# Optimization experiments

Measured on AMD Instinct MI355X. Metric: run time of the kernel, lower is better.

Reference implementation:

```python
import jax, jax.numpy as jnp
import numpy as np

VOCAB, D_MODEL, D_STATE, D_LATENT = 32000, 1024, 16, 32
SEQ, MAX_ITERS, TOL = 8192, 20, 1e-5


def _linear_params(k, out_d, in_d):
    lim = 1.0 / np.sqrt(in_d)  # eqx.nn.Linear default uniform init
    kw, kb = jax.random.split(k)
    W = jax.random.uniform(kw, (out_d, in_d), minval=-lim, maxval=lim, dtype=jnp.float32)
    b = jax.random.uniform(kb, (out_d,), minval=-lim, maxval=lim, dtype=jnp.float32)
    return W, b


def setup_inputs() -> dict:
    key = jax.random.key(0)
    ks = jax.random.split(key, 8)
    tokens = jax.random.randint(ks[0], (SEQ,), 0, VOCAB)
    emb = jax.random.normal(ks[1], (VOCAB, D_MODEL), dtype=jnp.float32) * 0.02
    Wf, bf = _linear_params(ks[2], D_LATENT // 2, D_STATE + D_MODEL)
    Wf2, bf2 = _linear_params(ks[3], D_LATENT // 2, D_STATE + D_MODEL)
    Wlam, blam = _linear_params(ks[4], D_STATE, D_LATENT + D_MODEL)
    Wu, bu = _linear_params(ks[5], D_STATE, D_LATENT + D_MODEL)
    Wout, bout = _linear_params(ks[6], D_MODEL, D_LATENT + D_STATE)
    return {"tokens": tokens, "emb": emb, "Wf": Wf, "bf": bf, "Wf2": Wf2, "bf2": bf2,
            "Wlam": Wlam, "blam": blam, "Wu": Wu, "bu": bu, "Wout": Wout, "bout": bout}


def reference(tokens, emb, Wf, bf, Wf2, bf2, Wlam, blam, Wu, bu, Wout, bout):
    x = emb[tokens]  # [S, d_model]

    def compute_lambda_u(z):
        zx = jnp.concatenate([z, x], axis=-1)              # [S, d_latent+d_model]
        lam = jax.nn.sigmoid(zx @ Wlam.T + blam)           # [S, d_state]
        u = zx @ Wu.T + bu                                 # [S, d_state]
        return lam, u

    def scan_h(lam, u):
        # h_t = lam_t * h_{t-1} + u_t via associative scan
        def binop(left, right):
            a1, b1 = left
            a2, b2 = right
            return (a1 * a2, a2 * b1 + b2)
        _, h = jax.lax.associative_scan(binop, (lam, u), axis=0)
        return h

    def f_theta(z, h_prev):
        hx = jnp.concatenate([h_prev, x], axis=-1)         # [S, d_state+d_model]
        alpha = jax.nn.sigmoid(hx @ Wf.T + bf)             # [S, d_latent//2]
        sigma = jax.nn.sigmoid(hx @ Wf2.T + bf2)
        u, v = jnp.split(z, 2, axis=-1)
        rho, beta, gamma = 30.0, 15.6, 0.26
        thresh = jnp.tanh(rho * (v - u))
        du = 1.0 - alpha * jnp.exp(beta * v) * (1.0 - gamma * (0.3 - u)) + sigma * thresh
        dv = -1.0 + alpha * jnp.exp(beta * u) * (1.0 + gamma * (0.3 - v)) + sigma * thresh
        return z + 0.001 * jnp.concatenate([du, dv], axis=-1)

    # Bounded fixed-point iteration with convergence freeze (emulates while_loop)
    def body(carry, _):
        z, z_prev, done = carry
        done = done | (jnp.linalg.norm(z - z_prev) < TOL)
        lam, u = compute_lambda_u(z)
        h = scan_h(lam, u)
        h_prev = jnp.concatenate([jnp.zeros((1, D_STATE), z.dtype), h[:-1]], axis=0)
        z_new = f_theta(z, h_prev)
        z_out = jnp.where(done, z, z_new)
        zp_out = jnp.where(done, z_prev, z)
        return (z_out, zp_out, done), None

    z0 = jnp.zeros((SEQ, D_LATENT), jnp.float32)
    zp0 = jnp.full((SEQ, D_LATENT), jnp.inf, jnp.float32)
    (z_star, _, _), _ = jax.lax.scan(body, (z0, zp0, jnp.array(False)), None, length=MAX_ITERS)

    lam, u = compute_lambda_u(z_star)
    h_star = scan_h(lam, u)
    zh = jnp.concatenate([z_star, h_star], axis=-1)        # [S, d_latent+d_state]
    return zh @ Wout.T + bout                              # [S, d_model]
```

## Files before the change

### kernel.cpp

```cpp
#include <hip/hip_runtime.h>

#define SEQ     8192
#define DM      1024
#define NB      256
#define CH      32
#define HALO    32
#define W       64
#define NT      1024
#define MAXITERS 20

__device__ __forceinline__ float sigmoidf(float x) {
    return 1.0f / (1.0f + __expf(-x));
}
__device__ __forceinline__ float tanh_fast(float x) {
    const float e = __expf(2.0f * x);
    return 1.0f - 2.0f / (e + 1.0f);
}
__device__ __forceinline__ float rl(float v, int lane) {
    return __uint_as_float(__builtin_amdgcn_readlane(__float_as_uint(v), lane));
}

__global__ __launch_bounds__(256) void k1_embed_proj(
    const int* __restrict__ tokens, const float* __restrict__ emb,
    const float* __restrict__ Wf,  const float* __restrict__ bf,
    const float* __restrict__ Wf2, const float* __restrict__ bf2,
    const float* __restrict__ Wlam,const float* __restrict__ blam,
    const float* __restrict__ Wu,  const float* __restrict__ bu,
    float* __restrict__ xlam, float* __restrict__ xu,
    float* __restrict__ xf,   float* __restrict__ xf2)
{
    __shared__ float4 xs4[8 * 256];
    const int tid = threadIdx.x;
    const int tokbase = blockIdx.x * 8;

    for (int j = tid; j < 8 * 256; j += 256) {
        const int tok = j >> 8, q = j & 255;
        const int row = tokens[tokbase + tok];
        const int qs = q ^ ((q >> 6) & 3);
        xs4[tok * 256 + qs] =
            *reinterpret_cast<const float4*>(emb + (size_t)row * DM + q * 4);
    }
    __syncthreads();

    const int r  = tid >> 2;
    const int kq = tid & 3;
    const int arr = r >> 4;
    const int c   = r & 15;

    const float* wb; const float* bv; float* dst; int wstr, woff;
    if (arr == 0)      { wb = Wlam; wstr = 1056; woff = 32; bv = blam; dst = xlam; }
    else if (arr == 1) { wb = Wu;   wstr = 1056; woff = 32; bv = bu;   dst = xu;   }
    else if (arr == 2) { wb = Wf;   wstr = 1040; woff = 16; bv = bf;   dst = xf;   }
    else               { wb = Wf2;  wstr = 1040; woff = 16; bv = bf2;  dst = xf2;  }

    const float4* wrow = reinterpret_cast<const float4*>(wb + (size_t)c * wstr + woff) + kq * 64;

    float2 a2[8];
    #pragma unroll
    for (int t = 0; t < 8; ++t) a2[t] = make_float2(0.f, 0.f);

    #pragma unroll 8
    for (int i = 0; i < 64; ++i) {
        const float4 w4 = wrow[i];
        const int gs = (kq * 64 + i) ^ kq;
        #pragma unroll
        for (int t = 0; t < 8; ++t) {
            const float4 x4 = xs4[t * 256 + gs];
            a2[t].x += w4.x * x4.x;  a2[t].y += w4.y * x4.y;
            a2[t].x += w4.z * x4.z;  a2[t].y += w4.w * x4.w;
        }
    }

    #pragma unroll
    for (int t = 0; t < 8; ++t) {
        float acc = a2[t].x + a2[t].y;
        acc += __shfl_xor(acc, 1);
        acc += __shfl_xor(acc, 2);
        if (kq == 0) {
            const float bz = bv[c];
            dst[(size_t)(tokbase + t) * 16 + c] = acc + bz;
        }
    }
}

__global__ __launch_bounds__(NT) void k2_fixed_point(
    const float* __restrict__ Wf,  const float* __restrict__ Wf2,
    const float* __restrict__ Wlam,const float* __restrict__ Wu,
    const float* __restrict__ xf,  const float* __restrict__ xf2,
    const float* __restrict__ xlam,const float* __restrict__ xu,
    const float* __restrict__ Wout,const float* __restrict__ bout,
    float* __restrict__ out)
{
    __shared__ float zsf[W * 32];
    __shared__ float hhT[16][W + 2];
    __shared__ float zhs[CH][48];

    const int tid = threadIdx.x;
    const int b = blockIdx.x;
    const int s0 = (b - 1) * CH;
    const int tl = tid & 63;
    const int c  = __builtin_amdgcn_readfirstlane(tid >> 6);

    for (int i = tid; i < W * 32; i += NT) zsf[i] = 0.0f;

    const float* WlamC = Wlam + (size_t)c * 1056;
    const float* WuC   = Wu   + (size_t)c * 1056;
    const float* WfC   = Wf   + (size_t)c * 1040;
    const float* Wf2C  = Wf2  + (size_t)c * 1040;
    const float w0 = (tl < 32) ? WlamC[tl] : WuC[tl - 32];
    const float w1 = (tl < 16) ? WfC[tl] : ((tl < 32) ? Wf2C[tl - 16] : 0.0f);

    const int gt = s0 + tl;
    const bool act = (gt >= 0);
    const size_t gi = (size_t)(act ? gt : 0) * 16 + c;
    const float xl = xlam[gi], xuv = xu[gi], xfv = xf[gi], x2v = xf2[gi];
    const int sw = tl & 7;
    __syncthreads();

    for (int r = 1; r <= MAXITERS + 1; ++r) {
        float accx = xl, accy = xuv;
        #pragma unroll
        for (int g = 0; g < 8; ++g) {
            const float4 z4 = *reinterpret_cast<const float4*>(
                &zsf[tl * 32 + ((g ^ sw) << 2)]);
            const int s0_ = 4 * g;
            const int j0 = ((s0_ + 0) & 1) ? 16 + ((s0_ + 0) >> 1) : ((s0_ + 0) >> 1);
            const int j1 = ((s0_ + 1) & 1) ? 16 + ((s0_ + 1) >> 1) : ((s0_ + 1) >> 1);
            const int j2 = ((s0_ + 2) & 1) ? 16 + ((s0_ + 2) >> 1) : ((s0_ + 2) >> 1);
            const int j3 = ((s0_ + 3) & 1) ? 16 + ((s0_ + 3) >> 1) : ((s0_ + 3) >> 1);
            accx += z4.x * rl(w0, j0);  accy += z4.x * rl(w0, 32 + j0);
            accx += z4.y * rl(w0, j1);  accy += z4.y * rl(w0, 32 + j1);
            accx += z4.z * rl(w0, j2);  accy += z4.z * rl(w0, 32 + j2);
            accx += z4.w * rl(w0, j3);  accy += z4.w * rl(w0, 32 + j3);
        }
        float A = act ? sigmoidf(accx) : 0.0f;
        float B = act ? accy : 0.0f;

        #pragma unroll
        for (int d = 1; d < 64; d <<= 1) {
            float pA = __shfl_up(A, d, 64);
            float pB = __shfl_up(B, d, 64);
            pA = (tl >= d) ? pA : 1.0f;
            pB = (tl >= d) ? pB : 0.0f;
            B = A * pB + B;
            A = A * pA;
        }
        hhT[c][tl] = B;
        __syncthreads();

        if (r == MAXITERS + 1) {
            for (int i = tid; i < CH * 48; i += NT) {
                const int tt = i / 48, j = i - tt * 48;
                const int tle = HALO + tt;
                float v;
                if (j < 32) {
                    const int s = (j < 16) ? 2 * j : 2 * (j - 16) + 1;
                    v = zsf[tle * 32 + ((((s >> 2) ^ (tle & 7)) << 2) | (s & 3))];
                } else {
                    v = hhT[j - 32][tle];
                }
                zhs[tt][j] = v;
            }
            __syncthreads();
            {
                const int col = tid;
                const float* wp = Wout + (size_t)col * 48;
                float4 wq[12];
                #pragma unroll
                for (int j = 0; j < 12; ++j)
                    wq[j] = *reinterpret_cast<const float4*>(wp + j * 4);
                const float bz = bout[col];
                for (int tt = 0; tt < CH; ++tt) {
                    float a = bz;
                    #pragma unroll
                    for (int j = 0; j < 12; ++j) {
                        const float4 z4 = *reinterpret_cast<const float4*>(&zhs[tt][j * 4]);
                        a += wq[j].x * z4.x + wq[j].y * z4.y
                           + wq[j].z * z4.z + wq[j].w * z4.w;
                    }
                    out[(size_t)(b * CH + tt) * 1024 + col] = a;
                }
            }
            break;
        }

        {
            const int tp = (tl == 0) ? 0 : tl - 1;
            float asx = xfv, asy = x2v;
            #pragma unroll
            for (int j = 0; j < 16; ++j) {
                const float hp = hhT[j][tp];
                asx += hp * rl(w1, j);
                asy += hp * rl(w1, 16 + j);
            }
            if (tl == 0) { asx = xfv; asy = x2v; }
            const float al_ = sigmoidf(asx);
            const float sg  = sigmoidf(asy);

            const int pos = tl * 32 + ((((c >> 1) ^ sw) << 2) | ((2 * c) & 3));
            float2 uv = *reinterpret_cast<const float2*>(&zsf[pos]);
            const float th = tanh_fast(30.0f * (uv.y - uv.x));
            const float du = 0.001f * ( 1.0f - al_ * __expf(15.6f * uv.y) * (1.0f - 0.26f * (0.3f - uv.x)) + sg * th);
            const float dv = 0.001f * (-1.0f + al_ * __expf(15.6f * uv.x) * (1.0f + 0.26f * (0.3f - uv.y)) + sg * th);
            if (act) {
                uv.x += du; uv.y += dv;
                *reinterpret_cast<float2*>(&zsf[pos]) = uv;
            }
        }
        __syncthreads();
    }
}

extern "C" void kernel_launch(void* const* d_in, const int* in_sizes, int n_in,
                              void* d_out, int out_size, void* d_ws, size_t ws_size,
                              hipStream_t stream) {
    (void)in_sizes; (void)n_in; (void)out_size; (void)ws_size;
    const int*   tokens = (const int*)  d_in[0];
    const float* emb    = (const float*)d_in[1];
    const float* Wf     = (const float*)d_in[2];
    const float* bf     = (const float*)d_in[3];
    const float* Wf2    = (const float*)d_in[4];
    const float* bf2    = (const float*)d_in[5];
    const float* Wlam   = (const float*)d_in[6];
    const float* blam   = (const float*)d_in[7];
    const float* Wu     = (const float*)d_in[8];
    const float* bu     = (const float*)d_in[9];
    const float* Wout   = (const float*)d_in[10];
    const float* bout   = (const float*)d_in[11];

    float* ws   = (float*)d_ws;
    float* xlam = ws;
    float* xu   = ws + 131072;
    float* xf   = ws + 262144;
    float* xf2  = ws + 393216;

    k1_embed_proj<<<SEQ / 8, 256, 0, stream>>>(tokens, emb, Wf, bf, Wf2, bf2,
                                               Wlam, blam, Wu, bu,
                                               xlam, xu, xf, xf2);

    k2_fixed_point<<<NB, NT, 0, stream>>>(Wf, Wf2, Wlam, Wu,
                                          xf, xf2, xlam, xu,
                                          Wout, bout, (float*)d_out);
}
```

Baseline: 130.6 us.

## Split output projection into separate kernel with more blocks

Moves the final zh @ Wout projection out of the fixed-point kernel into a new kernel. The fixed-point kernel now writes z and h to a workspace buffer, and the new kernel launches 512 blocks of 256 threads, each covering 16 tokens. This spreads the 32 MB output write across many more blocks than the 256 fixed-point blocks could use. It costs an extra launch and a small round trip through global memory for the intermediate.

```diff
diff --git a/kernel.cpp b/kernel.cpp
--- a/kernel.cpp
+++ b/kernel.cpp
@@ -88,12 +88,10 @@
     const float* __restrict__ Wlam,const float* __restrict__ Wu,
     const float* __restrict__ xf,  const float* __restrict__ xf2,
     const float* __restrict__ xlam,const float* __restrict__ xu,
-    const float* __restrict__ Wout,const float* __restrict__ bout,
-    float* __restrict__ out)
+    float* __restrict__ zhg)
 {
     __shared__ float zsf[W * 32];
     __shared__ float hhT[16][W + 2];
-    __shared__ float zhs[CH][48];
 
     const int tid = threadIdx.x;
     const int b = blockIdx.x;
@@ -159,27 +157,7 @@
                 } else {
                     v = hhT[j - 32][tle];
                 }
-                zhs[tt][j] = v;
-            }
-            __syncthreads();
-            {
-                const int col = tid;
-                const float* wp = Wout + (size_t)col * 48;
-                float4 wq[12];
-                #pragma unroll
-                for (int j = 0; j < 12; ++j)
-                    wq[j] = *reinterpret_cast<const float4*>(wp + j * 4);
-                const float bz = bout[col];
-                for (int tt = 0; tt < CH; ++tt) {
-                    float a = bz;
-                    #pragma unroll
-                    for (int j = 0; j < 12; ++j) {
-                        const float4 z4 = *reinterpret_cast<const float4*>(&zhs[tt][j * 4]);
-                        a += wq[j].x * z4.x + wq[j].y * z4.y
-                           + wq[j].z * z4.z + wq[j].w * z4.w;
-                    }
-                    out[(size_t)(b * CH + tt) * 1024 + col] = a;
-                }
+                zhg[(size_t)(b * CH + tt) * 48 + j] = v;
             }
             break;
         }
@@ -208,6 +186,41 @@
             }
         }
         __syncthreads();
+    }
+}
+
+__global__ __launch_bounds__(256) void k3_out(
+    const float* __restrict__ zhg, const float* __restrict__ Wout,
+    const float* __restrict__ bout, float* __restrict__ out)
+{
+    __shared__ float zh[16][48];
+    const int tid = threadIdx.x;
+    const int tb = blockIdx.x * 16;
+
+    for (int i = tid; i < 16 * 48; i += 256)
+        zh[i / 48][i % 48] = zhg[(size_t)tb * 48 + i];
+    __syncthreads();
+
+    #pragma unroll 1
+    for (int p = 0; p < 4; ++p) {
+        const int col = p * 256 + tid;
+        const float* wp = Wout + (size_t)col * 48;
+        float4 wq[12];
+        #pragma unroll
+        for (int j = 0; j < 12; ++j)
+            wq[j] = *reinterpret_cast<const float4*>(wp + j * 4);
+        const float bz = bout[col];
+        #pragma unroll 4
+        for (int tt = 0; tt < 16; ++tt) {
+            float a = bz;
+            #pragma unroll
+            for (int j = 0; j < 12; ++j) {
+                const float4 z4 = *reinterpret_cast<const float4*>(&zh[tt][j * 4]);
+                a += wq[j].x * z4.x + wq[j].y * z4.y
+                   + wq[j].z * z4.z + wq[j].w * z4.w;
+            }
+            out[(size_t)(tb + tt) * 1024 + col] = a;
+        }
     }
 }
 
@@ -233,12 +246,14 @@
     float* xu   = ws + 131072;
     float* xf   = ws + 262144;
     float* xf2  = ws + 393216;
+    float* zhg  = ws + 524288;
 
     k1_embed_proj<<<SEQ / 8, 256, 0, stream>>>(tokens, emb, Wf, bf, Wf2, bf2,
                                                Wlam, blam, Wu, bu,
                                                xlam, xu, xf, xf2);
 
     k2_fixed_point<<<NB, NT, 0, stream>>>(Wf, Wf2, Wlam, Wu,
-                                          xf, xf2, xlam, xu,
-                                          Wout, bout, (float*)d_out);
-}
+                                          xf, xf2, xlam, xu, zhg);
+
+    k3_out<<<SEQ / 16, 256, 0, stream>>>(zhg, Wout, bout, (float*)d_out);
+}
```

Result: no change. 130.8 us (+0.2%).
